# Optimization experiments

Measured on AMD Instinct MI355X. Metric: run time of the kernel, lower is better.

Reference implementation:

```python
import math
import jax, jax.numpy as jnp
import numpy as np

B, T, D, H, E, K = 2, 2048, 1024, 16, 8, 2
HD = D // H                      # head_dim = 64
CAP = math.ceil(1.25 * B * T / E)  # capacity per expert = 640
NEG = -1e9


def setup_inputs() -> dict:
    key = jax.random.key(0)
    ks = jax.random.split(key, 8)
    s = 0.02
    return {
        "x": jax.random.normal(ks[0], (B, T, D), jnp.float32),
        "ln1_g": jnp.ones((D,), jnp.float32),
        "ln1_b": jnp.zeros((D,), jnp.float32),
        "w_qkv": jax.random.normal(ks[1], (3 * D, D), jnp.float32) * s,
        "w_proj": jax.random.normal(ks[2], (D, D), jnp.float32) * s,
        "ln2_g": jnp.ones((D,), jnp.float32),
        "ln2_b": jnp.zeros((D,), jnp.float32),
        "w_gate": jax.random.normal(ks[3], (E, D), jnp.float32) * s,
        "w1": jax.random.normal(ks[4], (E, D, 4 * D), jnp.float32) * s,
        "b1": jnp.zeros((E, 4 * D), jnp.float32),
        "w2": jax.random.normal(ks[5], (E, 4 * D, D), jnp.float32) * s,
        "b2": jnp.zeros((E, D), jnp.float32),
    }


def _layernorm(x, g, b, eps=1e-5):
    m = x.mean(-1, keepdims=True)
    v = ((x - m) ** 2).mean(-1, keepdims=True)
    return (x - m) * jax.lax.rsqrt(v + eps) * g + b


def _rope(q, k):
    # q,k: [B,T,H,HD]; rotate-half RoPE with half_dim = HD//2 frequencies
    half = HD // 2
    pos = jnp.arange(T, dtype=jnp.float32)[:, None]
    inv_freq = 1.0 / (10000.0 ** (jnp.arange(0, HD, 2, dtype=jnp.float32) / HD))
    ang = pos * inv_freq                              # [T, half]
    sin = jnp.sin(ang)[None, :, None, :]
    cos = jnp.cos(ang)[None, :, None, :]

    def rot(t):
        t1, t2 = t[..., :half], t[..., half:]
        return jnp.concatenate([t1 * cos - t2 * sin, t1 * sin + t2 * cos], -1)

    return rot(q), rot(k)


def _attention(x, w_qkv, w_proj):
    qkv = (x @ w_qkv.T).reshape(B, T, H, 3 * HD)
    q, k, v = jnp.split(qkv, 3, axis=-1)              # each [B,T,H,HD]
    q, k = _rope(q, k)
    scores = jnp.einsum('bqhd,bkhd->bhqk', q, k) / math.sqrt(HD)
    causal = jnp.tril(jnp.ones((T, T), bool))
    scores = jnp.where(causal, scores, NEG)
    probs = jax.nn.softmax(scores, axis=-1)
    out = jnp.einsum('bhqk,bkhd->bqhd', probs, v).reshape(B, T, D)
    return out @ w_proj.T


def _sparse_moe(x2d, w_gate, w1, b1, w2, b2):
    # x2d: [N, D] flattened tokens. Eval mode: no noise, no dropout.
    N = x2d.shape[0]
    gates = jax.nn.softmax((x2d @ w_gate.T).astype(jnp.float32), axis=-1)  # [N,E]
    gate_vals, idx = jax.lax.top_k(gates, K)          # [N,K]
    gate_vals = gate_vals.astype(x2d.dtype)

    # Capacity enforcement: token order position within each expert
    mask = jnp.zeros((N, E), bool).at[jnp.arange(N)[:, None], idx].set(True)
    pos = jnp.cumsum(mask.astype(jnp.int32), axis=0) * mask - 1   # [N,E]
    keep = (pos < CAP) & mask
    slot = jnp.take_along_axis(pos, idx, axis=1)      # [N,K]
    kept = jnp.take_along_axis(keep, idx, axis=1)     # [N,K] bool

    # Dispatch: dropped tokens go to pad slot CAP (masked out at combine)
    slot_w = jnp.where(kept, slot, CAP).reshape(-1)   # [N*K]
    e_flat = idx.reshape(-1)                          # [N*K]
    xk = jnp.broadcast_to(x2d[:, None, :], (N, K, D)).reshape(-1, D)
    xk = xk * kept.reshape(-1, 1)
    buf = jnp.zeros((E, CAP + 1, D), x2d.dtype).at[e_flat, slot_w].set(xk)

    # Grouped expert MLP (GELU exact, matching nn.GELU default)
    h = jax.nn.gelu(jnp.einsum('ecd,edf->ecf', buf, w1) + b1[:, None, :],
                    approximate=False)
    out = jnp.einsum('ecf,efd->ecd', h, w2) + b2[:, None, :]

    # Combine: gather each token's expert output, weight by gate, mask drops
    y = out[e_flat, slot_w].reshape(N, K, D) * (gate_vals * kept)[..., None]
    return y.sum(axis=1)


def reference(x, ln1_g, ln1_b, w_qkv, w_proj, ln2_g, ln2_b,
              w_gate, w1, b1, w2, b2):
    h = x + _attention(_layernorm(x, ln1_g, ln1_b), w_qkv, w_proj)
    moe_in = _layernorm(h, ln2_g, ln2_b)
    moe_out = _sparse_moe(moe_in.reshape(B * T, D), w_gate, w1, b1, w2, b2)
    return h + moe_out.reshape(B, T, D)
```

## Files before the change

### kernel.cpp

```cpp
#include <hip/hip_runtime.h>
#include <hip/hip_bf16.h>

typedef __bf16 bf16;
typedef __attribute__((ext_vector_type(8))) __bf16 bf16x8;
typedef __attribute__((ext_vector_type(4))) __bf16 bf16x4;
typedef __attribute__((ext_vector_type(4))) float f32x4;
typedef __attribute__((ext_vector_type(16))) float f32x16;

#define NB 2
#define NT 2048
#define ND 1024
#define NH 16
#define HD_ 64
#define NE 8
#define NCAP 640
#define NTOK 4096
#define NDFF 4096

static __device__ __forceinline__ f32x4 mfma16(bf16x8 a, bf16x8 b, f32x4 c) {
  return __builtin_amdgcn_mfma_f32_16x16x32_bf16(a, b, c, 0, 0, 0);
}
static __device__ __forceinline__ f32x16 mfma32(bf16x8 a, bf16x8 b, f32x16 c) {
  return __builtin_amdgcn_mfma_f32_32x32x16_bf16(a, b, c, 0, 0, 0);
}
static __device__ __forceinline__ unsigned pk2(float a, float b) {
  union { __bf16 h[2]; unsigned u; } z;
  z.h[0] = (__bf16)a; z.h[1] = (__bf16)b;
  return z.u;
}
static __device__ __forceinline__ void gload_lds16(const bf16* g, bf16* l) {
  __builtin_amdgcn_global_load_lds(
      (const __attribute__((address_space(1))) unsigned int*)g,
      (__attribute__((address_space(3))) unsigned int*)l, 16, 0, 0);
}

__global__ __launch_bounds__(256) void cvt_k(const float* __restrict__ in,
                                             bf16* __restrict__ out, int n4) {
  int i = blockIdx.x * 256 + threadIdx.x;
  int stride = gridDim.x * 256;
  for (; i < n4; i += stride) {
    f32x4 v = ((const f32x4*)in)[i];
    bf16x4 o;
    o[0] = (bf16)v[0]; o[1] = (bf16)v[1]; o[2] = (bf16)v[2]; o[3] = (bf16)v[3];
    ((bf16x4*)out)[i] = o;
  }
}

__global__ __launch_bounds__(256) void transpose_k(const float* __restrict__ in,
                                                   bf16* __restrict__ out, int R, int C) {
  __shared__ float tile[64][65];
  const size_t zoff = (size_t)blockIdx.z * R * C;
  in += zoff; out += zoff;
  const int c0 = blockIdx.x * 64, r0 = blockIdx.y * 64;
  const int tx = threadIdx.x & 15, ty = threadIdx.x >> 4;
#pragma unroll
  for (int i = 0; i < 4; i++) {
    const int r = i * 16 + ty;
    f32x4 v = *(const f32x4*)(in + (size_t)(r0 + r) * C + c0 + tx * 4);
    *(f32x4*)&tile[r][tx * 4] = v;
  }
  __syncthreads();
#pragma unroll
  for (int i = 0; i < 4; i++) {
    const int rr = i * 16 + ty;
    bf16x4 o;
#pragma unroll
    for (int j = 0; j < 4; j++) o[j] = (bf16)tile[tx * 4 + j][rr];
    *(bf16x4*)(out + (size_t)(c0 + rr) * R + r0 + tx * 4) = o;
  }
}

__global__ __launch_bounds__(256) void transpose_v_k(const bf16* __restrict__ v,
                                                     bf16* __restrict__ vT) {
  __shared__ bf16 tile[32][33];
  int bh = blockIdx.z;
  const bf16* in = v + (size_t)bh * NT * HD_;
  bf16* out = vT + (size_t)bh * HD_ * NT;
  int t0 = blockIdx.x * 32, d0 = blockIdx.y * 32;
  int tx = threadIdx.x, ty = threadIdx.y;
#pragma unroll
  for (int i = 0; i < 4; i++)
    tile[ty + i * 8][tx] = in[(size_t)(t0 + ty + i * 8) * HD_ + d0 + tx];
  __syncthreads();
#pragma unroll
  for (int i = 0; i < 4; i++)
    out[(size_t)(d0 + ty + i * 8) * NT + t0 + tx] = tile[tx][ty + i * 8];
}

__global__ void rope_tab_k(float* __restrict__ tab) {
  int t = blockIdx.x, i = threadIdx.x;
  float inv = powf(10000.f, -(float)(2 * i) * (1.f / 64.f));
  float ang = (float)t * inv;
  float s, c;
  sincosf(ang, &s, &c);
  tab[(t * 32 + i) * 2] = s;
  tab[(t * 32 + i) * 2 + 1] = c;
}

template <bool BF16OUT>
__global__ __launch_bounds__(256) void ln_k(const float* __restrict__ in,
                                            const float* __restrict__ g,
                                            const float* __restrict__ bb,
                                            bf16* __restrict__ outb,
                                            float* __restrict__ outf) {
  const int row = blockIdx.x;
  const float* xr = in + (size_t)row * ND;
  const int tid = threadIdx.x, lane = tid & 63, wid = tid >> 6;
  f32x4 v = ((const f32x4*)xr)[tid];
  float s = v[0] + v[1] + v[2] + v[3];
  float sq = v[0] * v[0] + v[1] * v[1] + v[2] * v[2] + v[3] * v[3];
#pragma unroll
  for (int m = 1; m < 64; m <<= 1) {
    s += __shfl_xor(s, m, 64);
    sq += __shfl_xor(sq, m, 64);
  }
  __shared__ float red[8];
  if (lane == 0) { red[wid] = s; red[4 + wid] = sq; }
  __syncthreads();
  s = red[0] + red[1] + red[2] + red[3];
  sq = red[4] + red[5] + red[6] + red[7];
  float mean = s * (1.f / 1024.f);
  float var = sq * (1.f / 1024.f) - mean * mean;
  float rs = rsqrtf(var + 1e-5f);
#pragma unroll
  for (int c = 0; c < 4; c++) {
    int col = tid * 4 + c;
    float y = (v[c] - mean) * rs * g[col] + bb[col];
    if constexpr (BF16OUT) outb[(size_t)row * ND + col] = (bf16)y;
    else outf[(size_t)row * ND + col] = y;
  }
}

#define EPI_SPLIT_QKV 0
#define EPI_ADD_X 1
#define EPI_BIAS_GELU 2
#define EPI_STORE 3

template <int EPI, int STAGE, bool PAD>
__global__ __launch_bounds__(256) void gemm_bt_k(
    const bf16* __restrict__ A, const bf16* __restrict__ Bw,
    const int M, const int N, const int K, const int nsplit,
    const size_t zA, const size_t zB, const size_t zOut, const size_t zBias,
    const float* __restrict__ bias, const float* __restrict__ Xadd,
    void* __restrict__ Out, bf16* __restrict__ k_out, bf16* __restrict__ v_out) {
  const int z = blockIdx.z;
  const int ze = z / nsplit;
  const int kc = z - ze * nsplit;
  const int klen = K / nsplit;
  const int kb = kc * klen;
  const int nst = klen / 64;
  const int m0 = blockIdx.y * 128, n0 = blockIdx.x * 128;
  const int tid = threadIdx.x, lane = tid & 63, wid = tid >> 6;
  const int wm = (wid >> 1) * 64, wn = (wid & 1) * 64;
  const int l15 = lane & 15, ksl = lane >> 4;
  constexpr int LDB = (STAGE == 1 && PAD) ? 72 : 64;
  __shared__ __align__(16) bf16 As[128 * LDB];
  __shared__ __align__(16) bf16 Bs[128 * LDB];
  f32x4 acc[4][4];
#pragma unroll
  for (int i = 0; i < 4; i++)
#pragma unroll
    for (int j = 0; j < 4; j++) acc[i][j] = (f32x4){0.f, 0.f, 0.f, 0.f};

  if constexpr (STAGE == 0) {
    const int lr = lane >> 3, lc = (lane & 7) * 8;
    const bf16* Ag = A + zA * ze + (size_t)(m0 + wid * 32 + lr) * K + kb + lc;
    const bf16* Bg = Bw + zB * ze + (size_t)(n0 + wid * 32 + lr) * K + kb + lc;
    for (int s = 0; s < nst; ++s) {
      __syncthreads();
#pragma unroll
      for (int it = 0; it < 4; it++) {
        gload_lds16(Ag + (size_t)(it * 8) * K + s * 64, &As[(wid * 32 + it * 8) * 64]);
        gload_lds16(Bg + (size_t)(it * 8) * K + s * 64, &Bs[(wid * 32 + it * 8) * 64]);
      }
      __syncthreads();
#pragma unroll
      for (int kk = 0; kk < 2; kk++) {
        bf16x8 af[4], bfr[4];
        const int ko = kk * 32 + ksl * 8;
#pragma unroll
        for (int i = 0; i < 4; i++)
          af[i] = *(const bf16x8*)&As[(wm + i * 16 + l15) * 64 + ko];
#pragma unroll
        for (int j = 0; j < 4; j++)
          bfr[j] = *(const bf16x8*)&Bs[(wn + j * 16 + l15) * 64 + ko];
#pragma unroll
        for (int i = 0; i < 4; i++)
#pragma unroll
          for (int j = 0; j < 4; j++)
            acc[i][j] = mfma16(af[i], bfr[j], acc[i][j]);
      }
    }
  } else {
    const int sr = tid >> 3, sc = (tid & 7) * 8;
    const bf16* Ag = A + zA * ze + (size_t)(m0 + sr) * K + kb + sc;
    const bf16* Bg = Bw + zB * ze + (size_t)(n0 + sr) * K + kb + sc;
    bf16x8 av[4], bv[4];
#pragma unroll
    for (int it = 0; it < 4; it++) {
      av[it] = *(const bf16x8*)(Ag + (size_t)(it * 32) * K);
      bv[it] = *(const bf16x8*)(Bg + (size_t)(it * 32) * K);
    }
    for (int s = 0; s < nst; ++s) {
      __syncthreads();
#pragma unroll
      for (int it = 0; it < 4; it++) {
        *(bf16x8*)&As[(sr + it * 32) * LDB + sc] = av[it];
        *(bf16x8*)&Bs[(sr + it * 32) * LDB + sc] = bv[it];
      }
      __syncthreads();
      if (s + 1 < nst) {
#pragma unroll
        for (int it = 0; it < 4; it++) {
          av[it] = *(const bf16x8*)(Ag + (size_t)(it * 32) * K + (s + 1) * 64);
          bv[it] = *(const bf16x8*)(Bg + (size_t)(it * 32) * K + (s + 1) * 64);
        }
      }
#pragma unroll
      for (int kk = 0; kk < 2; kk++) {
        bf16x8 af[4], bfr[4];
        const int ko = kk * 32 + ksl * 8;
#pragma unroll
        for (int i = 0; i < 4; i++)
          af[i] = *(const bf16x8*)&As[(wm + i * 16 + l15) * LDB + ko];
#pragma unroll
        for (int j = 0; j < 4; j++)
          bfr[j] = *(const bf16x8*)&Bs[(wn + j * 16 + l15) * LDB + ko];
#pragma unroll
        for (int i = 0; i < 4; i++)
#pragma unroll
          for (int j = 0; j < 4; j++)
            acc[i][j] = mfma16(af[i], bfr[j], acc[i][j]);
      }
    }
  }

#pragma unroll
  for (int i = 0; i < 4; i++) {
#pragma unroll
    for (int j = 0; j < 4; j++) {
      const int mb = m0 + wm + i * 16 + ksl * 4;
      const int nc = n0 + wn + j * 16 + l15;
#pragma unroll
      for (int r = 0; r < 4; r++) {
        const int mr = mb + r;
        float vacc = acc[i][j][r];
        if constexpr (EPI == EPI_SPLIT_QKV) {
          const int h = nc / 192;
          const int rr = nc - h * 192;
          const int which = rr >> 6;
          const int d = rr & 63;
          const int b = mr >> 11, t = mr & 2047;
          bf16* dst = (which == 0) ? (bf16*)Out : (which == 1 ? k_out : v_out);
          dst[(((size_t)(b * NH + h)) * NT + t) * HD_ + d] = (bf16)vacc;
        } else if constexpr (EPI == EPI_ADD_X) {
          ((float*)Out)[(size_t)mr * N + nc] = vacc + Xadd[(size_t)mr * N + nc];
        } else if constexpr (EPI == EPI_BIAS_GELU) {
          float x = vacc + bias[zBias * ze + nc];
          float u2 = x * (2.3020882f + 0.10294772f * x * x);
          float gl = x * __builtin_amdgcn_rcpf(1.f + exp2f(-u2));
          ((bf16*)Out)[zOut * ze + (size_t)mr * N + nc] = (bf16)gl;
        } else {
          ((bf16*)Out)[((size_t)kc * NE + ze) * zOut + (size_t)mr * N + nc] = (bf16)vacc;
        }
      }
    }
  }
}

__global__ __launch_bounds__(256) void rope_k(bf16* __restrict__ q, bf16* __restrict__ k,
                                              const float* __restrict__ tab) {
  const int bh = blockIdx.y;
  const int t = blockIdx.x * 4 + (threadIdx.x >> 6);
  const int d = threadIdx.x & 63;
  const size_t row = ((size_t)bh * NT + t) * HD_;
  const int i = d & 31;
  const float sn = tab[(t * 32 + i) * 2], cs = tab[(t * 32 + i) * 2 + 1];
  {
    float a = (float)q[row + d];
    float b2 = (float)q[row + (d ^ 32)];
    float o = (d < 32) ? (a * cs - b2 * sn) : (b2 * sn + a * cs);
    q[row + d] = (bf16)(o * 0.18033688011112042f);
  }
  {
    float a = (float)k[row + d];
    float b2 = (float)k[row + (d ^ 32)];
    float o = (d < 32) ? (a * cs - b2 * sn) : (b2 * sn + a * cs);
    k[row + d] = (bf16)o;
  }
}

__global__ __launch_bounds__(256) void attn_k(const bf16* __restrict__ q,
                                              const bf16* __restrict__ k,
                                              const bf16* __restrict__ vT,
                                              bf16* __restrict__ attn_out) {
  __shared__ __align__(16) bf16 Kt[64 * 64];
  __shared__ __align__(16) bf16 Vt[64 * 64];
  const int bid = blockIdx.x;
  const int bh = bid & 31;
  const int ti = (bid >> 5) & 7;
  const int qt = (bid >> 8) ? (15 - ti) : ti;
  const int q0 = qt * 128;
  const int tid = threadIdx.x, lane = tid & 63, wid = tid >> 6;
  const int l31 = lane & 31, hi = lane >> 5;
  const int q0w = q0 + wid * 32;
  const int qrow = q0w + l31;
  const size_t base = (size_t)bh * (NT * HD_);
  const size_t baseT = (size_t)bh * (HD_ * NT);

  bf16x8 qf[4];
#pragma unroll
  for (int ks = 0; ks < 4; ks++)
    qf[ks] = *(const bf16x8*)(q + base + (size_t)qrow * HD_ + ks * 16 + hi * 8);

  f32x16 ot0, ot1;
#pragma unroll
  for (int r = 0; r < 16; r++) { ot0[r] = 0.f; ot1[r] = 0.f; }
  float m2 = -1e30f, l = 0.f;

  const int ntiles = qt * 2 + 2;
  const int swz = (l31 & 7);
  const int strow = tid >> 3, stc = tid & 7;
  const int cw0 = ((stc ^ (strow & 7)) * 8);
  bf16x8 kr[2], vr[2];
#pragma unroll
  for (int rr = 0; rr < 2; rr++) {
    kr[rr] = *(const bf16x8*)(k + base + (size_t)(strow + rr * 32) * HD_ + stc * 8);
    vr[rr] = *(const bf16x8*)(vT + baseT + (size_t)(strow + rr * 32) * NT + stc * 8);
  }

  for (int t = 0; t < ntiles; t++) {
    const int kv0 = t * 64;
    __syncthreads();
#pragma unroll
    for (int rr = 0; rr < 2; rr++) {
      *(bf16x8*)&Kt[(strow + rr * 32) * 64 + cw0] = kr[rr];
      *(bf16x8*)&Vt[(strow + rr * 32) * 64 + cw0] = vr[rr];
    }
    __syncthreads();
    if (t + 1 < ntiles) {
      const int kn = kv0 + 64;
#pragma unroll
      for (int rr = 0; rr < 2; rr++) {
        kr[rr] = *(const bf16x8*)(k + base + (size_t)(kn + strow + rr * 32) * HD_ + stc * 8);
        vr[rr] = *(const bf16x8*)(vT + baseT + (size_t)(strow + rr * 32) * NT + kn + stc * 8);
      }
    }
    if (kv0 > q0w + 31) continue;

    f32x16 s0, s1;
#pragma unroll
    for (int r = 0; r < 16; r++) { s0[r] = 0.f; s1[r] = 0.f; }
#pragma unroll
    for (int ks = 0; ks < 4; ks++) {
      const int cw = (((ks * 2 + hi) ^ swz) * 8);
      bf16x8 ka0 = *(const bf16x8*)&Kt[l31 * 64 + cw];
      bf16x8 ka1 = *(const bf16x8*)&Kt[(l31 + 32) * 64 + cw];
      s0 = mfma32(ka0, qf[ks], s0);
      s1 = mfma32(ka1, qf[ks], s1);
    }

    float p[32];
#pragma unroll
    for (int r = 0; r < 16; r++) { p[r] = s0[r]; p[16 + r] = s1[r]; }
    if (kv0 + 63 > q0w) {
#pragma unroll
      for (int sub = 0; sub < 2; sub++)
#pragma unroll
        for (int r = 0; r < 16; r++) {
          int kvg = kv0 + sub * 32 + (r & 3) + 8 * (r >> 2) + 4 * hi;
          if (kvg > qrow) p[sub * 16 + r] = -1e30f;
        }
    }
    float tm = p[0];
#pragma unroll
    for (int r = 1; r < 32; r++) tm = fmaxf(tm, p[r]);
    tm = fmaxf(tm, __shfl_xor(tm, 32, 64));
    if (!__all(tm <= m2 + 8.f)) {
      float mn = fmaxf(m2, tm);
      float sf = exp2f(m2 - mn);
      m2 = mn;
      l *= sf;
#pragma unroll
      for (int r = 0; r < 16; r++) { ot0[r] *= sf; ot1[r] *= sf; }
    }
    float ts = 0.f;
#pragma unroll
    for (int r = 0; r < 32; r++) { p[r] = exp2f(p[r] - m2); ts += p[r]; }
    ts += __shfl_xor(ts, 32, 64);
    l += ts;

#pragma unroll
    for (int ks = 0; ks < 4; ks++) {
      const int i0 = (ks >> 1) * 16 + (ks & 1) * 8;
      unsigned Aw = pk2(p[i0 + 0], p[i0 + 1]);
      unsigned Bw = pk2(p[i0 + 2], p[i0 + 3]);
      unsigned Cw = pk2(p[i0 + 4], p[i0 + 5]);
      unsigned Dw = pk2(p[i0 + 6], p[i0 + 7]);
      unsigned xA = (unsigned)__shfl_xor((int)Aw, 32, 64);
      unsigned xB = (unsigned)__shfl_xor((int)Bw, 32, 64);
      unsigned xC = (unsigned)__shfl_xor((int)Cw, 32, 64);
      unsigned xD = (unsigned)__shfl_xor((int)Dw, 32, 64);
      union { unsigned u[4]; bf16x8 v; } pa;
      pa.u[0] = hi ? xC : Aw;
      pa.u[1] = hi ? xD : Bw;
      pa.u[2] = hi ? Cw : xA;
      pa.u[3] = hi ? Dw : xB;
      const int cw = (((ks * 2 + hi) ^ swz) * 8);
      bf16x8 va0 = *(const bf16x8*)&Vt[l31 * 64 + cw];
      bf16x8 va1 = *(const bf16x8*)&Vt[(l31 + 32) * 64 + cw];
      ot0 = mfma32(va0, pa.v, ot0);
      ot1 = mfma32(va1, pa.v, ot1);
    }
  }

  const int b = bh >> 4, h = bh & 15;
  const float inv = 1.f / l;
  const size_t orow = ((size_t)(b * NT + qrow)) * ND + h * 64;
#pragma unroll
  for (int g = 0; g < 4; g++) {
    bf16x4 w0, w1;
#pragma unroll
    for (int c = 0; c < 4; c++) {
      w0[c] = (bf16)(ot0[g * 4 + c] * inv);
      w1[c] = (bf16)(ot1[g * 4 + c] * inv);
    }
    *(bf16x4*)(attn_out + orow + g * 8 + 4 * hi) = w0;
    *(bf16x4*)(attn_out + orow + 32 + g * 8 + 4 * hi) = w1;
  }
}

__global__ __launch_bounds__(256) void gate_k(const float* __restrict__ moe_in,
                                              const float* __restrict__ w_gate,
                                              int* __restrict__ idx, float* __restrict__ gv) {
  __shared__ float wg[8 * 1024];
  for (int i = threadIdx.x; i < 8192; i += 256) wg[i] = w_gate[i];
  __syncthreads();
  const int lane = threadIdx.x & 63, wid = threadIdx.x >> 6;
  for (int tt = 0; tt < 4; tt++) {
    const int n = blockIdx.x * 16 + wid * 4 + tt;
    const float* xr = moe_in + (size_t)n * ND;
    float a[8];
#pragma unroll
    for (int e = 0; e < 8; e++) a[e] = 0.f;
    for (int d0 = lane * 4; d0 < 1024; d0 += 256) {
      f32x4 xv = *(const f32x4*)(xr + d0);
#pragma unroll
      for (int e = 0; e < 8; e++) {
        const float* wr = &wg[e * 1024 + d0];
        a[e] += xv[0] * wr[0] + xv[1] * wr[1] + xv[2] * wr[2] + xv[3] * wr[3];
      }
    }
#pragma unroll
    for (int e = 0; e < 8; e++)
#pragma unroll
      for (int m = 1; m < 64; m <<= 1) a[e] += __shfl_xor(a[e], m, 64);
    if (lane == 0) {
      float mx = a[0];
#pragma unroll
      for (int e = 1; e < 8; e++) mx = fmaxf(mx, a[e]);
      float p[8], se = 0.f;
#pragma unroll
      for (int e = 0; e < 8; e++) { p[e] = expf(a[e] - mx); se += p[e]; }
      float inv = 1.f / se;
#pragma unroll
      for (int e = 0; e < 8; e++) p[e] *= inv;
      int i1 = 0; float v1 = p[0];
#pragma unroll
      for (int e = 1; e < 8; e++) if (p[e] > v1) { v1 = p[e]; i1 = e; }
      int i2 = -1; float v2 = -1.f;
#pragma unroll
      for (int e = 0; e < 8; e++) if (e != i1 && p[e] > v2) { v2 = p[e]; i2 = e; }
      idx[n * 2] = i1; idx[n * 2 + 1] = i2;
      gv[n * 2] = v1; gv[n * 2 + 1] = v2;
    }
  }
}

__global__ void scan_k(const int* __restrict__ idx, int* __restrict__ slot,
                       int* __restrict__ kept) {
  const int lane = threadIdx.x;
  int base[8];
#pragma unroll
  for (int e = 0; e < 8; e++) base[e] = 0;
  const unsigned long long lm = (lane == 63) ? ~0ull : ((1ull << (lane + 1)) - 1);
  for (int c = 0; c < 64; c++) {
    const int n = c * 64 + lane;
    const int e0 = idx[n * 2], e1 = idx[n * 2 + 1];
    int s0 = 0, s1 = 0;
#pragma unroll
    for (int e = 0; e < 8; e++) {
      unsigned long long m0 = __ballot(e0 == e);
      unsigned long long m1 = __ballot(e1 == e);
      unsigned long long m = m0 | m1;
      int pref = __popcll(m & lm);
      if (e0 == e) s0 = base[e] + pref - 1;
      if (e1 == e) s1 = base[e] + pref - 1;
      base[e] += __popcll(m);
    }
    slot[n * 2] = s0; slot[n * 2 + 1] = s1;
    kept[n * 2] = (s0 < NCAP) ? 1 : 0;
    kept[n * 2 + 1] = (s1 < NCAP) ? 1 : 0;
  }
}

__global__ __launch_bounds__(64) void scatter_k(const float* __restrict__ moe_in,
                                                const int* __restrict__ idx,
                                                const int* __restrict__ slot,
                                                const int* __restrict__ kept,
                                                bf16* __restrict__ buf) {
  const int a = blockIdx.x;
  if (!kept[a]) return;
  const int n = a >> 1;
  const int e = idx[a], s = slot[a];
  const float* src = moe_in + (size_t)n * ND;
  bf16* dst = buf + ((size_t)e * NCAP + s) * ND;
  for (int c = threadIdx.x * 4; c < 1024; c += 256) {
    f32x4 v = *(const f32x4*)(src + c);
    bf16x4 o;
    o[0] = (bf16)v[0]; o[1] = (bf16)v[1]; o[2] = (bf16)v[2]; o[3] = (bf16)v[3];
    *(bf16x4*)(dst + c) = o;
  }
}

__global__ __launch_bounds__(256) void gather_k(const float* __restrict__ h,
                                                const bf16* __restrict__ eout,
                                                const int* __restrict__ idx,
                                                const int* __restrict__ slot,
                                                const int* __restrict__ kept,
                                                const float* __restrict__ gv,
                                                const float* __restrict__ b2,
                                                float* __restrict__ out) {
  const size_t PS = (size_t)NE * NCAP * ND;
  const int n = blockIdx.x;
  const int k0 = kept[n * 2], k1 = kept[n * 2 + 1];
  const int i0 = idx[n * 2], i1 = idx[n * 2 + 1];
  const float g0 = k0 ? gv[n * 2] : 0.f;
  const float g1 = k1 ? gv[n * 2 + 1] : 0.f;
  const size_t r0 = k0 ? ((size_t)i0 * NCAP + slot[n * 2]) * ND : 0;
  const size_t r1 = k1 ? ((size_t)i1 * NCAP + slot[n * 2 + 1]) * ND : 0;
  const int c = threadIdx.x * 4;
  f32x4 o = *(const f32x4*)(h + (size_t)n * ND + c);
  if (k0) {
    bf16x4 ea = *(const bf16x4*)(eout + r0 + c);
    bf16x4 eb = *(const bf16x4*)(eout + PS + r0 + c);
    f32x4 bb = *(const f32x4*)(b2 + i0 * ND + c);
#pragma unroll
    for (int cc = 0; cc < 4; cc++)
      o[cc] += g0 * ((float)ea[cc] + (float)eb[cc] + bb[cc]);
  }
  if (k1) {
    bf16x4 ea = *(const bf16x4*)(eout + r1 + c);
    bf16x4 eb = *(const bf16x4*)(eout + PS + r1 + c);
    f32x4 bb = *(const f32x4*)(b2 + i1 * ND + c);
#pragma unroll
    for (int cc = 0; cc < 4; cc++)
      o[cc] += g1 * ((float)ea[cc] + (float)eb[cc] + bb[cc]);
  }
  *(f32x4*)(out + (size_t)n * ND + c) = o;
}

extern "C" void kernel_launch(void* const* d_in, const int* in_sizes, int n_in,
                              void* d_out, int out_size, void* d_ws, size_t ws_size,
                              hipStream_t stream) {
  (void)in_sizes; (void)n_in; (void)out_size;
  const float* x      = (const float*)d_in[0];
  const float* ln1_g  = (const float*)d_in[1];
  const float* ln1_b  = (const float*)d_in[2];
  const float* w_qkv  = (const float*)d_in[3];
  const float* w_proj = (const float*)d_in[4];
  const float* ln2_g  = (const float*)d_in[5];
  const float* ln2_b  = (const float*)d_in[6];
  const float* w_gate = (const float*)d_in[7];
  const float* w1     = (const float*)d_in[8];
  const float* b1     = (const float*)d_in[9];
  const float* w2     = (const float*)d_in[10];
  const float* b2     = (const float*)d_in[11];
  float* out = (float*)d_out;

  char* ws = (char*)d_ws;
  size_t off = 0;
  auto alloc = [&](size_t bytes) -> char* {
    char* p = ws + off;
    off += (bytes + 255) & ~(size_t)255;
    return p;
  };
  bf16* w1t    = (bf16*)alloc((size_t)NE * NDFF * ND * 2);
  bf16* w2t    = (bf16*)alloc((size_t)NE * ND * NDFF * 2);
  bf16* wqkvb  = (bf16*)alloc((size_t)3 * ND * ND * 2);
  bf16* wprojb = (bf16*)alloc((size_t)ND * ND * 2);
  float* hbufr = (float*)alloc((size_t)NTOK * ND * 4);
  float* moein = (float*)alloc((size_t)NTOK * ND * 4);
  float* ropet = (float*)alloc((size_t)NT * 32 * 2 * 4);
  int*   idx   = (int*)alloc((size_t)NTOK * 2 * 4);
  int*   slot  = (int*)alloc((size_t)NTOK * 2 * 4);
  int*   kept  = (int*)alloc((size_t)NTOK * 2 * 4);
  float* gv    = (float*)alloc((size_t)NTOK * 2 * 4);
  char*  S     = alloc((size_t)62914560);
  if (off > ws_size) return;

  const size_t MB8 = (size_t)8388608;
  bf16* xn    = (bf16*)(S);
  bf16* qp    = (bf16*)(S + MB8);
  bf16* kp    = (bf16*)(S + 2 * MB8);
  bf16* vp    = (bf16*)(S + 3 * MB8);
  bf16* attnp = (bf16*)(S + 4 * MB8);
  bf16* vTp   = (bf16*)(S);
  bf16* hbuf  = (bf16*)(S);
  bf16* buf   = (bf16*)(S + (size_t)41943040);
  bf16* eout  = (bf16*)(S + (size_t)41943040);

  dim3 tb(32, 8);
  cvt_k<<<2048, 256, 0, stream>>>(w_qkv, wqkvb, 3 * ND * ND / 4);
  cvt_k<<<1024, 256, 0, stream>>>(w_proj, wprojb, ND * ND / 4);
  transpose_k<<<dim3(NDFF / 64, ND / 64, NE), 256, 0, stream>>>(w1, w1t, ND, NDFF);
  transpose_k<<<dim3(ND / 64, NDFF / 64, NE), 256, 0, stream>>>(w2, w2t, NDFF, ND);
  rope_tab_k<<<NT, 32, 0, stream>>>(ropet);
  ln_k<true><<<NTOK, 256, 0, stream>>>(x, ln1_g, ln1_b, xn, nullptr);
  gemm_bt_k<EPI_SPLIT_QKV, 0, false><<<dim3(3 * ND / 128, NTOK / 128, 1), 256, 0, stream>>>(
      xn, wqkvb, NTOK, 3 * ND, ND, 1, 0, 0, 0, 0, nullptr, nullptr, qp, kp, vp);
  transpose_v_k<<<dim3(NT / 32, HD_ / 32, NB * NH), tb, 0, stream>>>(vp, vTp);
  rope_k<<<dim3(NT / 4, NB * NH), 256, 0, stream>>>(qp, kp, ropet);
  attn_k<<<512, 256, 0, stream>>>(qp, kp, vTp, attnp);
  gemm_bt_k<EPI_ADD_X, 1, true><<<dim3(ND / 128, NTOK / 128, 1), 256, 0, stream>>>(
      attnp, wprojb, NTOK, ND, ND, 1, 0, 0, 0, 0, nullptr, x, hbufr, nullptr, nullptr);
  ln_k<false><<<NTOK, 256, 0, stream>>>(hbufr, ln2_g, ln2_b, nullptr, moein);
  gate_k<<<NTOK / 16, 256, 0, stream>>>(moein, w_gate, idx, gv);
  scan_k<<<1, 64, 0, stream>>>(idx, slot, kept);
  scatter_k<<<NTOK * 2, 64, 0, stream>>>(moein, idx, slot, kept, buf);
  gemm_bt_k<EPI_BIAS_GELU, 0, false><<<dim3(NDFF / 128, NCAP / 128, NE), 256, 0, stream>>>(
      buf, w1t, NCAP, NDFF, ND, 1, (size_t)NCAP * ND, (size_t)NDFF * ND,
      (size_t)NCAP * NDFF, NDFF, b1, nullptr, hbuf, nullptr, nullptr);
  gemm_bt_k<EPI_STORE, 1, true><<<dim3(ND / 128, NCAP / 128, NE * 2), 256, 0, stream>>>(
      hbuf, w2t, NCAP, ND, NDFF, 2, (size_t)NCAP * NDFF, (size_t)ND * NDFF,
      (size_t)NCAP * ND, 0, nullptr, nullptr, eout, nullptr, nullptr);
  gather_k<<<NTOK, 256, 0, stream>>>(hbufr, eout, idx, slot, kept, gv, b2, out);
}
```

Measured before the change: 457.1 us.

## Fuse LN2 with gating, swizzle expert GEMM blocks per XCD, use exact erf GELU

Merges the second layernorm and the gate softmax/top-2 into one kernel, so moe_in is no longer re-read and the separate gate launch is gone. The split-K factor becomes a template parameter, and the two expert GEMMs get a block-index remap that spreads consecutive blocks across the 8 XCDs so neighbouring tiles share an XCD's L2. The GELU epilogue swaps the sigmoid-based approximation for exact erf, which matches the reference more closely but costs more ALU work per element.

```diff
diff --git a/kernel.cpp b/kernel.cpp
--- a/kernel.cpp
+++ b/kernel.cpp
@@ -97,12 +97,10 @@
   tab[(t * 32 + i) * 2 + 1] = c;
 }
 
-template <bool BF16OUT>
 __global__ __launch_bounds__(256) void ln_k(const float* __restrict__ in,
                                             const float* __restrict__ g,
                                             const float* __restrict__ bb,
-                                            bf16* __restrict__ outb,
-                                            float* __restrict__ outf) {
+                                            bf16* __restrict__ outb) {
   const int row = blockIdx.x;
   const float* xr = in + (size_t)row * ND;
   const int tid = threadIdx.x, lane = tid & 63, wid = tid >> 6;
@@ -126,8 +124,78 @@
   for (int c = 0; c < 4; c++) {
     int col = tid * 4 + c;
     float y = (v[c] - mean) * rs * g[col] + bb[col];
-    if constexpr (BF16OUT) outb[(size_t)row * ND + col] = (bf16)y;
-    else outf[(size_t)row * ND + col] = y;
+    outb[(size_t)row * ND + col] = (bf16)y;
+  }
+}
+
+__global__ __launch_bounds__(256) void ln_gate_k(const float* __restrict__ in,
+                                                 const float* __restrict__ g,
+                                                 const float* __restrict__ bb,
+                                                 const float* __restrict__ w_gate,
+                                                 float* __restrict__ moein,
+                                                 int* __restrict__ idx,
+                                                 float* __restrict__ gv) {
+  const int row = blockIdx.x;
+  const float* xr = in + (size_t)row * ND;
+  const int tid = threadIdx.x, lane = tid & 63, wid = tid >> 6;
+  f32x4 v = ((const f32x4*)xr)[tid];
+  float s = v[0] + v[1] + v[2] + v[3];
+  float sq = v[0] * v[0] + v[1] * v[1] + v[2] * v[2] + v[3] * v[3];
+#pragma unroll
+  for (int m = 1; m < 64; m <<= 1) {
+    s += __shfl_xor(s, m, 64);
+    sq += __shfl_xor(sq, m, 64);
+  }
+  __shared__ float red[8];
+  if (lane == 0) { red[wid] = s; red[4 + wid] = sq; }
+  __syncthreads();
+  s = red[0] + red[1] + red[2] + red[3];
+  sq = red[4] + red[5] + red[6] + red[7];
+  float mean = s * (1.f / 1024.f);
+  float var = sq * (1.f / 1024.f) - mean * mean;
+  float rs = rsqrtf(var + 1e-5f);
+  f32x4 y;
+#pragma unroll
+  for (int c = 0; c < 4; c++) {
+    int col = tid * 4 + c;
+    y[c] = (v[c] - mean) * rs * g[col] + bb[col];
+  }
+  *(f32x4*)(moein + (size_t)row * ND + tid * 4) = y;
+  float a[8];
+#pragma unroll
+  for (int e = 0; e < 8; e++) {
+    f32x4 wv = *(const f32x4*)(w_gate + e * ND + tid * 4);
+    a[e] = y[0] * wv[0] + y[1] * wv[1] + y[2] * wv[2] + y[3] * wv[3];
+  }
+#pragma unroll
+  for (int e = 0; e < 8; e++)
+#pragma unroll
+    for (int m = 1; m < 64; m <<= 1) a[e] += __shfl_xor(a[e], m, 64);
+  __shared__ float red2[4][8];
+  if (lane < 8) red2[wid][lane] = a[lane];
+  __syncthreads();
+  if (tid == 0) {
+    float t[8];
+#pragma unroll
+    for (int e = 0; e < 8; e++)
+      t[e] = red2[0][e] + red2[1][e] + red2[2][e] + red2[3][e];
+    float mx = t[0];
+#pragma unroll
+    for (int e = 1; e < 8; e++) mx = fmaxf(mx, t[e]);
+    float p[8], se = 0.f;
+#pragma unroll
+    for (int e = 0; e < 8; e++) { p[e] = expf(t[e] - mx); se += p[e]; }
+    float inv = 1.f / se;
+#pragma unroll
+    for (int e = 0; e < 8; e++) p[e] *= inv;
+    int i1 = 0; float v1 = p[0];
+#pragma unroll
+    for (int e = 1; e < 8; e++) if (p[e] > v1) { v1 = p[e]; i1 = e; }
+    int i2 = -1; float v2 = -1.f;
+#pragma unroll
+    for (int e = 0; e < 8; e++) if (e != i1 && p[e] > v2) { v2 = p[e]; i2 = e; }
+    idx[row * 2] = i1; idx[row * 2 + 1] = i2;
+    gv[row * 2] = v1; gv[row * 2 + 1] = v2;
   }
 }
 
@@ -136,20 +204,32 @@
 #define EPI_BIAS_GELU 2
 #define EPI_STORE 3
 
-template <int EPI, int STAGE, bool PAD>
+template <int EPI, int STAGE, bool PAD, int NSPLIT, bool MSWZ>
 __global__ __launch_bounds__(256) void gemm_bt_k(
     const bf16* __restrict__ A, const bf16* __restrict__ Bw,
-    const int M, const int N, const int K, const int nsplit,
+    const int M, const int N, const int K,
     const size_t zA, const size_t zB, const size_t zOut, const size_t zBias,
     const float* __restrict__ bias, const float* __restrict__ Xadd,
     void* __restrict__ Out, bf16* __restrict__ k_out, bf16* __restrict__ v_out) {
-  const int z = blockIdx.z;
-  const int ze = z / nsplit;
-  const int kc = z - ze * nsplit;
-  const int klen = K / nsplit;
+  int bx = blockIdx.x, by = blockIdx.y, bz = blockIdx.z;
+  if constexpr (MSWZ) {
+    const int gx = gridDim.x, gy = gridDim.y;
+    int lin = bx + gx * (by + gy * bz);
+    int xcd = lin & 7;
+    int t = lin >> 3;
+    by = t % gy;
+    int gq = t / gy;
+    int gg = gq * 8 + xcd;
+    bx = gg % gx;
+    bz = gg / gx;
+  }
+  const int z = bz;
+  const int ze = z / NSPLIT;
+  const int kc = z % NSPLIT;
+  const int klen = K / NSPLIT;
   const int kb = kc * klen;
   const int nst = klen / 64;
-  const int m0 = blockIdx.y * 128, n0 = blockIdx.x * 128;
+  const int m0 = by * 128, n0 = bx * 128;
   const int tid = threadIdx.x, lane = tid & 63, wid = tid >> 6;
   const int wm = (wid >> 1) * 64, wn = (wid & 1) * 64;
   const int l15 = lane & 15, ksl = lane >> 4;
@@ -257,8 +337,7 @@
           ((float*)Out)[(size_t)mr * N + nc] = vacc + Xadd[(size_t)mr * N + nc];
         } else if constexpr (EPI == EPI_BIAS_GELU) {
           float x = vacc + bias[zBias * ze + nc];
-          float u2 = x * (2.3020882f + 0.10294772f * x * x);
-          float gl = x * __builtin_amdgcn_rcpf(1.f + exp2f(-u2));
+          float gl = 0.5f * x * (1.f + erff(x * 0.70710678118654752f));
           ((bf16*)Out)[zOut * ze + (size_t)mr * N + nc] = (bf16)gl;
         } else {
           ((bf16*)Out)[((size_t)kc * NE + ze) * zOut + (size_t)mr * N + nc] = (bf16)vacc;
@@ -427,53 +506,6 @@
     }
     *(bf16x4*)(attn_out + orow + g * 8 + 4 * hi) = w0;
     *(bf16x4*)(attn_out + orow + 32 + g * 8 + 4 * hi) = w1;
-  }
-}
-
-__global__ __launch_bounds__(256) void gate_k(const float* __restrict__ moe_in,
-                                              const float* __restrict__ w_gate,
-                                              int* __restrict__ idx, float* __restrict__ gv) {
-  __shared__ float wg[8 * 1024];
-  for (int i = threadIdx.x; i < 8192; i += 256) wg[i] = w_gate[i];
-  __syncthreads();
-  const int lane = threadIdx.x & 63, wid = threadIdx.x >> 6;
-  for (int tt = 0; tt < 4; tt++) {
-    const int n = blockIdx.x * 16 + wid * 4 + tt;
-    const float* xr = moe_in + (size_t)n * ND;
-    float a[8];
-#pragma unroll
-    for (int e = 0; e < 8; e++) a[e] = 0.f;
-    for (int d0 = lane * 4; d0 < 1024; d0 += 256) {
-      f32x4 xv = *(const f32x4*)(xr + d0);
-#pragma unroll
-      for (int e = 0; e < 8; e++) {
-        const float* wr = &wg[e * 1024 + d0];
-        a[e] += xv[0] * wr[0] + xv[1] * wr[1] + xv[2] * wr[2] + xv[3] * wr[3];
-      }
-    }
-#pragma unroll
-    for (int e = 0; e < 8; e++)
-#pragma unroll
-      for (int m = 1; m < 64; m <<= 1) a[e] += __shfl_xor(a[e], m, 64);
-    if (lane == 0) {
-      float mx = a[0];
-#pragma unroll
-      for (int e = 1; e < 8; e++) mx = fmaxf(mx, a[e]);
-      float p[8], se = 0.f;
-#pragma unroll
-      for (int e = 0; e < 8; e++) { p[e] = expf(a[e] - mx); se += p[e]; }
-      float inv = 1.f / se;
-#pragma unroll
-      for (int e = 0; e < 8; e++) p[e] *= inv;
-      int i1 = 0; float v1 = p[0];
-#pragma unroll
-      for (int e = 1; e < 8; e++) if (p[e] > v1) { v1 = p[e]; i1 = e; }
-      int i2 = -1; float v2 = -1.f;
-#pragma unroll
-      for (int e = 0; e < 8; e++) if (e != i1 && p[e] > v2) { v2 = p[e]; i2 = e; }
-      idx[n * 2] = i1; idx[n * 2 + 1] = i2;
-      gv[n * 2] = v1; gv[n * 2 + 1] = v2;
-    }
   }
 }
 
@@ -616,23 +648,26 @@
   transpose_k<<<dim3(NDFF / 64, ND / 64, NE), 256, 0, stream>>>(w1, w1t, ND, NDFF);
   transpose_k<<<dim3(ND / 64, NDFF / 64, NE), 256, 0, stream>>>(w2, w2t, NDFF, ND);
   rope_tab_k<<<NT, 32, 0, stream>>>(ropet);
-  ln_k<true><<<NTOK, 256, 0, stream>>>(x, ln1_g, ln1_b, xn, nullptr);
-  gemm_bt_k<EPI_SPLIT_QKV, 0, false><<<dim3(3 * ND / 128, NTOK / 128, 1), 256, 0, stream>>>(
-      xn, wqkvb, NTOK, 3 * ND, ND, 1, 0, 0, 0, 0, nullptr, nullptr, qp, kp, vp);
+  ln_k<<<NTOK, 256, 0, stream>>>(x, ln1_g, ln1_b, xn);
+  gemm_bt_k<EPI_SPLIT_QKV, 0, false, 1, false>
+      <<<dim3(3 * ND / 128, NTOK / 128, 1), 256, 0, stream>>>(
+      xn, wqkvb, NTOK, 3 * ND, ND, 0, 0, 0, 0, nullptr, nullptr, qp, kp, vp);
   transpose_v_k<<<dim3(NT / 32, HD_ / 32, NB * NH), tb, 0, stream>>>(vp, vTp);
   rope_k<<<dim3(NT / 4, NB * NH), 256, 0, stream>>>(qp, kp, ropet);
   attn_k<<<512, 256, 0, stream>>>(qp, kp, vTp, attnp);
-  gemm_bt_k<EPI_ADD_X, 1, true><<<dim3(ND / 128, NTOK / 128, 1), 256, 0, stream>>>(
-      attnp, wprojb, NTOK, ND, ND, 1, 0, 0, 0, 0, nullptr, x, hbufr, nullptr, nullptr);
-  ln_k<false><<<NTOK, 256, 0, stream>>>(hbufr, ln2_g, ln2_b, nullptr, moein);
-  gate_k<<<NTOK / 16, 256, 0, stream>>>(moein, w_gate, idx, gv);
+  gemm_bt_k<EPI_ADD_X, 1, true, 1, false>
+      <<<dim3(ND / 128, NTOK / 128, 1), 256, 0, stream>>>(
+      attnp, wprojb, NTOK, ND, ND, 0, 0, 0, 0, nullptr, x, hbufr, nullptr, nullptr);
+  ln_gate_k<<<NTOK, 256, 0, stream>>>(hbufr, ln2_g, ln2_b, w_gate, moein, idx, gv);
   scan_k<<<1, 64, 0, stream>>>(idx, slot, kept);
   scatter_k<<<NTOK * 2, 64, 0, stream>>>(moein, idx, slot, kept, buf);
-  gemm_bt_k<EPI_BIAS_GELU, 0, false><<<dim3(NDFF / 128, NCAP / 128, NE), 256, 0, stream>>>(
-      buf, w1t, NCAP, NDFF, ND, 1, (size_t)NCAP * ND, (size_t)NDFF * ND,
+  gemm_bt_k<EPI_BIAS_GELU, 0, false, 1, true>
+      <<<dim3(NDFF / 128, NCAP / 128, NE), 256, 0, stream>>>(
+      buf, w1t, NCAP, NDFF, ND, (size_t)NCAP * ND, (size_t)NDFF * ND,
       (size_t)NCAP * NDFF, NDFF, b1, nullptr, hbuf, nullptr, nullptr);
-  gemm_bt_k<EPI_STORE, 1, true><<<dim3(ND / 128, NCAP / 128, NE * 2), 256, 0, stream>>>(
-      hbuf, w2t, NCAP, ND, NDFF, 2, (size_t)NCAP * NDFF, (size_t)ND * NDFF,
+  gemm_bt_k<EPI_STORE, 1, true, 2, true>
+      <<<dim3(ND / 128, NCAP / 128, NE * 2), 256, 0, stream>>>(
+      hbuf, w2t, NCAP, ND, NDFF, (size_t)NCAP * NDFF, (size_t)ND * NDFF,
       (size_t)NCAP * ND, 0, nullptr, nullptr, eout, nullptr, nullptr);
   gather_k<<<NTOK, 256, 0, stream>>>(hbufr, eout, idx, slot, kept, gv, b2, out);
 }
```

Result: faster. 443.4 us, median of 2 (-3.0%).
